# Optimization experiments

Measured on AMD Instinct MI355X. Metric: run time of the kernel, lower is better.

## Reference

```python
import jax, jax.numpy as jnp
import numpy as np

B, N, C = 8, 8192, 512
H, DH = 8, C // 8
SCALE = 0.02


def setup_inputs() -> dict:
    key = jax.random.key(0)
    k0, k1, k2, k3, k4 = jax.random.split(key, 5)
    return {
        "x": jax.random.normal(k0, (B, N, C), dtype=jnp.float32),
        "w1": SCALE * jax.random.normal(k1, (2, H, DH, DH), dtype=jnp.float32),
        "b1": SCALE * jax.random.normal(k2, (2, H, DH), dtype=jnp.float32),
        "w2": SCALE * jax.random.normal(k3, (2, H, DH, DH), dtype=jnp.float32),
        "b2": SCALE * jax.random.normal(k4, (2, H, DH), dtype=jnp.float32),
    }


def reference(x, w1, b1, w2, b2):
    dtype = x.dtype
    x = x.astype(jnp.float32)
    b, n, c = x.shape
    xf = jnp.fft.rfft(x, axis=1, norm="ortho")            # [B, N//2+1, C] complex
    xf = xf.reshape(b, n // 2 + 1, H, DH)                  # [B, F, H, DH]
    xr, xi = jnp.real(xf), jnp.imag(xf)
    # per-head complex linear 1 + GELU (complex mult split into real/imag)
    o1r = jax.nn.gelu(
        jnp.einsum("bfhi,hio->bfho", xr, w1[0])
        - jnp.einsum("bfhi,hio->bfho", xi, w1[1]) + b1[0], approximate=False)
    o1i = jax.nn.gelu(
        jnp.einsum("bfhi,hio->bfho", xi, w1[0])
        + jnp.einsum("bfhi,hio->bfho", xr, w1[1]) + b1[1], approximate=False)
    # per-head complex linear 2
    o2r = (jnp.einsum("bfhi,hio->bfho", o1r, w2[0])
           - jnp.einsum("bfhi,hio->bfho", o1i, w2[1]) + b2[0])
    o2i = (jnp.einsum("bfhi,hio->bfho", o1i, w2[0])
           + jnp.einsum("bfhi,hio->bfho", o1r, w2[1]) + b2[1])
    yf = (o2r + 1j * o2i).reshape(b, n // 2 + 1, c)
    y = jnp.fft.irfft(yf, n=n, axis=1, norm="ortho")
    return y.astype(dtype)
```

## Files before the change

### kernel.cpp

```cpp
#include <hip/hip_runtime.h>
#include <math.h>

#define BB    8
#define NLEN  8192
#define CC    512
#define HH    8
#define DH    64
#define MH    4096
#define FREQ  4097
#define FP    4160
#define NSEQ  (BB*CC)

#define REGION_BYTES ((size_t)NSEQ * FP * 4ull)

static __device__ __align__(256) unsigned char g_scratch[2ull * (size_t)NSEQ * FP * 4ull];
__device__ unsigned short g_wprep[8 * 4 * 64 * 64];

typedef __attribute__((ext_vector_type(8))) short bf16x8;
typedef __attribute__((ext_vector_type(4))) float f32x4;
typedef __attribute__((ext_vector_type(4))) unsigned u32x4;

__device__ __forceinline__ f32x4 MFMA(bf16x8 a, bf16x8 b, f32x4 c){
  return __builtin_amdgcn_mfma_f32_16x16x32_bf16(a, b, c, 0, 0, 0);
}

__device__ __forceinline__ unsigned short f2bf(float f){
  unsigned u = __float_as_uint(f);
  return (unsigned short)((u + 0x7fffu + ((u >> 16) & 1u)) >> 16);
}
__device__ __forceinline__ unsigned pack2(float a, float b){
  return (unsigned)f2bf(a) | ((unsigned)f2bf(b) << 16);
}
__device__ __forceinline__ float bflo(unsigned u){ return __uint_as_float(u << 16); }
__device__ __forceinline__ float bfhi(unsigned u){ return __uint_as_float(u & 0xffff0000u); }

__device__ const float C32C[16] = {
  1.f, 0.98078528f, 0.92387953f, 0.83146961f, 0.70710678f, 0.55557023f,
  0.38268343f, 0.19509032f, 0.f, -0.19509032f, -0.38268343f, -0.55557023f,
  -0.70710678f, -0.83146961f, -0.92387953f, -0.98078528f};
__device__ const float C32S[16] = {
  0.f, 0.19509032f, 0.38268343f, 0.55557023f, 0.70710678f, 0.83146961f,
  0.92387953f, 0.98078528f, 1.f, 0.98078528f, 0.92387953f, 0.83146961f,
  0.70710678f, 0.55557023f, 0.38268343f, 0.19509032f};

__device__ __forceinline__ float gelu_fast(float v){
  float x  = v * 0.70710678118654752440f;
  float ax = fabsf(x);
  float t  = __builtin_amdgcn_rcpf(fmaf(0.3275911f, ax, 1.0f));
  float p  = fmaf(fmaf(fmaf(fmaf(1.061405429f, t, -1.453152027f), t,
                            1.421413741f), t, -0.284496736f), t, 0.254829592f);
  float e  = __expf(-x * x);
  float erf_ax = fmaf(-p * t, e, 1.0f);
  float erfx = copysignf(erf_ax, x);
  return 0.5f * v * (1.0f + erfx);
}

__device__ __forceinline__ float2 cadd(float2 a, float2 b){ return make_float2(a.x+b.x, a.y+b.y); }
__device__ __forceinline__ float2 csub(float2 a, float2 b){ return make_float2(a.x-b.x, a.y-b.y); }
__device__ __forceinline__ float2 cmul(float2 a, float2 b){
  return make_float2(fmaf(a.x, b.x, -(a.y*b.y)), fmaf(a.x, b.y, a.y*b.x));
}

__global__ __launch_bounds__(256) void transpose_in_k(const float* __restrict__ in,
                                                      unsigned* __restrict__ out){
  __shared__ float tile[64][33];
  int b  = blockIdx.z;
  int c0 = blockIdx.x * 32;
  int n0 = blockIdx.y * 64;
  int t  = threadIdx.x;
  int tx = t & 31, ty = t >> 5;
  const float* src = in + ((size_t)b * NLEN + n0) * CC + c0;
  #pragma unroll
  for (int k = 0; k < 8; ++k)
    tile[ty + 8*k][tx] = src[(size_t)(ty + 8*k) * CC + tx];
  __syncthreads();
  int lt = t & 15;
  int nl = 4 * lt;
  #pragma unroll
  for (int kk = 0; kk < 2; ++kk){
    int cl = (t >> 4) + 16*kk;
    uint2 u;
    u.x = pack2(tile[nl    ][cl], tile[nl + 1][cl]);
    u.y = pack2(tile[nl + 2][cl], tile[nl + 3][cl]);
    *(uint2*)(out + ((size_t)(b * CC + c0 + cl) * NLEN + n0) / 2 + 2*lt) = u;
  }
}

__global__ __launch_bounds__(256) void transpose_out_k(const unsigned* __restrict__ in,
                                                       float* __restrict__ out){
  __shared__ float tile[64][33];
  int b  = blockIdx.z;
  int c0 = blockIdx.x * 32;
  int n0 = blockIdx.y * 64;
  int t  = threadIdx.x;
  int lt = t & 15;
  int nl = 4 * lt;
  #pragma unroll
  for (int kk = 0; kk < 2; ++kk){
    int cl = (t >> 4) + 16*kk;
    uint2 u = *(const uint2*)(in + ((size_t)(b * CC + c0 + cl) * NLEN + n0) / 2 + 2*lt);
    tile[nl    ][cl] = bflo(u.x);
    tile[nl + 1][cl] = bfhi(u.x);
    tile[nl + 2][cl] = bflo(u.y);
    tile[nl + 3][cl] = bfhi(u.y);
  }
  __syncthreads();
  int tx = t & 31, ty = t >> 5;
  float* dst = out + ((size_t)b * NLEN + n0) * CC + c0;
  #pragma unroll
  for (int k = 0; k < 8; ++k)
    dst[(size_t)(ty + 8*k) * CC + tx] = tile[ty + 8*k][tx];
}

#define SL(e) ((e) + ((e) >> 4))
#define PERM16(p) ((((p) & 3) << 2) | ((p) >> 2))

template<int SIGN>
__device__ __forceinline__ void dft4ip(float2& v0, float2& v1, float2& v2, float2& v3){
  float2 s02 = cadd(v0, v2), d02 = csub(v0, v2);
  float2 s13 = cadd(v1, v3), d13 = csub(v1, v3);
  float2 id = make_float2(-(float)SIGN * d13.y, (float)SIGN * d13.x);
  v0 = cadd(s02, s13);
  v1 = cadd(d02, id);
  v2 = csub(s02, s13);
  v3 = csub(d02, id);
}

template<int SIGN>
__device__ __forceinline__ float2 w16c(int m){
  const float c1 = 0.9238795325112867f, s1 = 0.3826834323650898f, r = 0.7071067811865476f;
  float cs = 1.f, sn = 0.f;
  if (m == 1){ cs = c1;  sn = s1; }
  else if (m == 2){ cs = r;   sn = r; }
  else if (m == 3){ cs = s1;  sn = c1; }
  else if (m == 4){ cs = 0.f; sn = 1.f; }
  else if (m == 6){ cs = -r;  sn = r; }
  else if (m == 9){ cs = -c1; sn = -s1; }
  return make_float2(cs, (float)SIGN * sn);
}

template<int SIGN>
__device__ __forceinline__ void dft16ip(float2 v[16]){
  #pragma unroll
  for (int q0 = 0; q0 < 4; ++q0) dft4ip<SIGN>(v[q0], v[q0+4], v[q0+8], v[q0+12]);
  #pragma unroll
  for (int p0 = 0; p0 < 4; ++p0)
    #pragma unroll
    for (int q0 = 0; q0 < 4; ++q0){
      const int m = p0 * q0;
      if (m) v[q0 + 4*p0] = cmul(v[q0 + 4*p0], w16c<SIGN>(m));
    }
  #pragma unroll
  for (int p0 = 0; p0 < 4; ++p0) dft4ip<SIGN>(v[4*p0], v[4*p0+1], v[4*p0+2], v[4*p0+3]);
}

template<int SIGN>
__device__ __forceinline__ void twiddle16(float2 v[16], int jm, float invRNs){
  float ang = (float)SIGN * 6.2831853071795864769f * (float)jm * invRNs;
  float sn, cs; __sincosf(ang, &sn, &cs);
  float2 tw[16];
  tw[1] = make_float2(cs, sn);
  #pragma unroll
  for (int q = 2; q < 16; ++q) tw[q] = cmul(tw[q >> 1], tw[q - (q >> 1)]);
  #pragma unroll
  for (int q = 1; q < 16; ++q) v[q] = cmul(v[q], tw[q]);
}

template<int SIGN, int NS>
__device__ __forceinline__ void fft_mid_pass(float2* lds2, float2 v[16], int t){
  #pragma unroll
  for (int q = 0; q < 16; ++q) v[q] = lds2[SL(t + 256*q)];
  int jm = t & (NS - 1);
  if (NS > 1) twiddle16<SIGN>(v, jm, 1.0f / (16.0f * (float)NS));
  dft16ip<SIGN>(v);
  __syncthreads();
  int base = ((t - jm) << 4) + jm;
  #pragma unroll
  for (int p = 0; p < 16; ++p) lds2[SL(base + p*NS)] = v[PERM16(p)];
  __syncthreads();
}

#define ORTHO_S 0.011048543456039806f

__global__ __launch_bounds__(256) void fft_fwd_k(const unsigned* __restrict__ xt,
                                                 unsigned* __restrict__ spec){
  __shared__ float2 lds2[4352];
  int t = threadIdx.x;
  size_t row = blockIdx.x;
  const unsigned* src = xt + row * (NLEN/2);
  float2 v[16];
  #pragma unroll
  for (int q = 0; q < 16; ++q){
    unsigned u = src[t + 256*q];
    v[q] = make_float2(bflo(u), bfhi(u));
  }
  dft16ip<-1>(v);
  #pragma unroll
  for (int p = 0; p < 16; ++p) lds2[SL(16*t + p)] = v[PERM16(p)];
  __syncthreads();
  fft_mid_pass<-1, 16 >(lds2, v, t);
  fft_mid_pass<-1, 256>(lds2, v, t);
  unsigned* dst = spec + row * (size_t)FP;
  float snb, csb;
  __sincosf(-6.2831853071795864769f * (float)t / (float)NLEN, &snb, &csb);
  #pragma unroll
  for (int q = 0; q < 8; ++q){
    int k = t + 256*q;
    float2 zk = lds2[SL(k)];
    float2 zc = lds2[SL((MH - k) & (MH - 1))];
    float ex = 0.5f*(zk.x + zc.x);
    float ey = 0.5f*(zk.y - zc.y);
    float ox =  0.5f*(zk.y + zc.y);
    float oy = -0.5f*(zk.x - zc.x);
    float cs = fmaf(csb, C32C[q],  snb*C32S[q]);
    float sn = fmaf(snb, C32C[q], -csb*C32S[q]);
    float P = cs*ox - sn*oy;
    float Q = cs*oy + sn*ox;
    dst[k]      = pack2(ORTHO_S*(ex + P), ORTHO_S*(ey + Q));
    dst[MH - k] = pack2(ORTHO_S*(ex - P), ORTHO_S*(Q - ey));
  }
  if (t == 0){
    float2 zm = lds2[SL(2048)];
    dst[2048] = pack2(ORTHO_S*zm.x, -ORTHO_S*zm.y);
  }
}

__global__ __launch_bounds__(256) void fft_inv_k(const unsigned* __restrict__ spec,
                                                 unsigned* __restrict__ yt){
  __shared__ float2 lds2[4352];
  int t = threadIdx.x;
  size_t row = blockIdx.x;
  const unsigned* src = spec + row * (size_t)FP;
  float snb, csb;
  __sincosf(6.2831853071795864769f * (float)t / (float)NLEN, &snb, &csb);
  #pragma unroll
  for (int q = 0; q < 8; ++q){
    int k = t + 256*q;
    unsigned uk = src[k];
    unsigned uc = src[MH - k];
    float2 xk = make_float2(bflo(uk), bfhi(uk));
    float2 xc = make_float2(bflo(uc), bfhi(uc));
    if (k == 0){ xk.y = 0.0f; xc.y = 0.0f; }
    float ex = xk.x + xc.x;
    float ey = xk.y - xc.y;
    float dx = xk.x - xc.x;
    float dy = xk.y + xc.y;
    float cs = fmaf(csb, C32C[q], -snb*C32S[q]);
    float sn = fmaf(snb, C32C[q],  csb*C32S[q]);
    float ox = cs*dx - sn*dy;
    float oy = cs*dy + sn*dx;
    lds2[SL(k)] = make_float2(ex - oy, ey + ox);
    if (k > 0)
      lds2[SL(MH - k)] = make_float2(ex + oy, ox - ey);
  }
  if (t == 0){
    unsigned um = src[2048];
    lds2[SL(2048)] = make_float2(2.0f*bflo(um), -2.0f*bfhi(um));
  }
  __syncthreads();
  float2 v[16];
  fft_mid_pass<1, 1  >(lds2, v, t);
  fft_mid_pass<1, 16 >(lds2, v, t);
  fft_mid_pass<1, 256>(lds2, v, t);
  uint4* d4 = (uint4*)(yt + row * (NLEN/2) + 16*t);
  #pragma unroll
  for (int g = 0; g < 4; ++g){
    float2 w0 = lds2[SL(16*t + 4*g    )];
    float2 w1 = lds2[SL(16*t + 4*g + 1)];
    float2 w2 = lds2[SL(16*t + 4*g + 2)];
    float2 w3 = lds2[SL(16*t + 4*g + 3)];
    uint4 stv;
    stv.x = pack2(ORTHO_S*w0.x, ORTHO_S*w0.y);
    stv.y = pack2(ORTHO_S*w1.x, ORTHO_S*w1.y);
    stv.z = pack2(ORTHO_S*w2.x, ORTHO_S*w2.y);
    stv.w = pack2(ORTHO_S*w3.x, ORTHO_S*w3.y);
    d4[g] = stv;
  }
}

__global__ __launch_bounds__(256) void wprep_k(const float* __restrict__ w1,
                                               const float* __restrict__ w2){
  int t = threadIdx.x;
  int h = blockIdx.x;
  #pragma unroll 4
  for (int u = 0; u < 64; ++u){
    int idx = t + 256*u;
    int p = idx >> 12;
    int o = (idx >> 6) & 63;
    int jj = idx & 63;
    int swo = (o ^ (o >> 3)) & 7;
    int s = (((jj >> 3) ^ swo) << 3) | (jj & 7);
    int i;
    if (p < 2){
      i = s;
    } else {
      int ks = s >> 5, g = (s >> 3) & 3, j = s & 7;
      i = (2*ks + (j >> 2))*16 + 4*g + (j & 3);
    }
    const float* src = (p < 2) ? w1 : w2;
    float v = src[(size_t)(p & 1) * 32768 + (size_t)h * 4096 + i * 64 + o];
    g_wprep[(size_t)h * 16384 + idx] = f2bf(v);
  }
}

__global__ __launch_bounds__(256) void afno_mid_mfma_k(const unsigned* __restrict__ spec_in,
                                                       unsigned* __restrict__ spec_out,
                                                       const float* __restrict__ b1,
                                                       const float* __restrict__ b2){
  __shared__ unsigned short Wl[16384];
  const int t = threadIdx.x;
  const int bx = blockIdx.x, h = blockIdx.y, b = blockIdx.z;
  const int F0 = bx * 64;
  const size_t rowbase = ((size_t)b * HH + h) * DH;
  const int l = t & 63, wv = t >> 6;
  const int lf = l & 15, lg = l >> 4;
  const int wf0 = wv * 16;

  int f = F0 + wf0 + lf;
  int fc = (f < FP) ? f : (FP - 1);
  const unsigned* xcol = spec_in + rowbase * (size_t)FP + fc;
  unsigned bins[16];
  #pragma unroll
  for (int ks = 0; ks < 2; ++ks){
    int i0 = (ks*4 + lg) * 8;
    #pragma unroll
    for (int j = 0; j < 8; ++j)
      bins[ks*8 + j] = xcol[(i0 + j) * FP];
  }

  {
    const uint4* gw  = (const uint4*)(g_wprep + (size_t)h * 16384);
    uint4*       sw4 = (uint4*)Wl;
    #pragma unroll
    for (int u = 0; u < 8; ++u) sw4[t + 256*u] = gw[t + 256*u];
  }
  float4 br1[4], bi1[4];
  #pragma unroll
  for (int mt = 0; mt < 4; ++mt){
    br1[mt] = *(const float4*)(b1 +       (size_t)h*64 + mt*16 + lg*4);
    bi1[mt] = *(const float4*)(b1 + 512 + (size_t)h*64 + mt*16 + lg*4);
  }
  float b2r[4], b2i[4];
  #pragma unroll
  for (int nt = 0; nt < 4; ++nt){
    b2r[nt] = b2[(size_t)h*64 + nt*16 + lf];
    b2i[nt] = b2[512 + (size_t)h*64 + nt*16 + lf];
  }
  __syncthreads();

  const unsigned short* W1R = Wl;
  const unsigned short* W1I = Wl + 4096;
  const unsigned short* W2R = Wl + 8192;
  const unsigned short* W2I = Wl + 12288;
  const f32x4 zz = {0.f, 0.f, 0.f, 0.f};

  f32x4 a1R[4], a1I[4];
  #pragma unroll
  for (int mt = 0; mt < 4; ++mt){ a1R[mt] = zz; a1I[mt] = zz; }

  #pragma unroll
  for (int ks = 0; ks < 2; ++ks){
    u32x4 pr, pi;
    pr.x = __builtin_amdgcn_perm(bins[ks*8+1], bins[ks*8+0], 0x05040100u);
    pr.y = __builtin_amdgcn_perm(bins[ks*8+3], bins[ks*8+2], 0x05040100u);
    pr.z = __builtin_amdgcn_perm(bins[ks*8+5], bins[ks*8+4], 0x05040100u);
    pr.w = __builtin_amdgcn_perm(bins[ks*8+7], bins[ks*8+6], 0x05040100u);
    pi.x = __builtin_amdgcn_perm(bins[ks*8+1], bins[ks*8+0], 0x07060302u);
    pi.y = __builtin_amdgcn_perm(bins[ks*8+3], bins[ks*8+2], 0x07060302u);
    pi.z = __builtin_amdgcn_perm(bins[ks*8+5], bins[ks*8+4], 0x07060302u);
    pi.w = __builtin_amdgcn_perm(bins[ks*8+7], bins[ks*8+6], 0x07060302u);
    bf16x8 bxr = __builtin_bit_cast(bf16x8, pr);
    bf16x8 bxi = __builtin_bit_cast(bf16x8, pi);
    int b0 = ks*4 + lg;
    #pragma unroll
    for (int mt = 0; mt < 4; ++mt){
      int o = mt*16 + lf;
      int swo = (o ^ (o >> 3)) & 7;
      int off = o*64 + ((b0 ^ swo) << 3);
      bf16x8 awr  = *(const bf16x8*)(W1R + off);
      bf16x8 awi  = *(const bf16x8*)(W1I + off);
      bf16x8 awin = awi ^ (short)0x8000;
      a1R[mt] = MFMA(awr,  bxr, a1R[mt]);
      a1R[mt] = MFMA(awin, bxi, a1R[mt]);
      a1I[mt] = MFMA(awi,  bxr, a1I[mt]);
      a1I[mt] = MFMA(awr,  bxi, a1I[mt]);
    }
  }

  bf16x8 aFr[2], aFi[2], aFin[2];
  #pragma unroll
  for (int ks = 0; ks < 2; ++ks){
    const int m0 = 2*ks, m1 = 2*ks + 1;
    u32x4 wr4, wi4;
    wr4.x = pack2(gelu_fast(a1R[m0][0] + br1[m0].x), gelu_fast(a1R[m0][1] + br1[m0].y));
    wr4.y = pack2(gelu_fast(a1R[m0][2] + br1[m0].z), gelu_fast(a1R[m0][3] + br1[m0].w));
    wr4.z = pack2(gelu_fast(a1R[m1][0] + br1[m1].x), gelu_fast(a1R[m1][1] + br1[m1].y));
    wr4.w = pack2(gelu_fast(a1R[m1][2] + br1[m1].z), gelu_fast(a1R[m1][3] + br1[m1].w));
    wi4.x = pack2(gelu_fast(a1I[m0][0] + bi1[m0].x), gelu_fast(a1I[m0][1] + bi1[m0].y));
    wi4.y = pack2(gelu_fast(a1I[m0][2] + bi1[m0].z), gelu_fast(a1I[m0][3] + bi1[m0].w));
    wi4.z = pack2(gelu_fast(a1I[m1][0] + bi1[m1].x), gelu_fast(a1I[m1][1] + bi1[m1].y));
    wi4.w = pack2(gelu_fast(a1I[m1][2] + bi1[m1].z), gelu_fast(a1I[m1][3] + bi1[m1].w));
    aFr[ks]  = __builtin_bit_cast(bf16x8, wr4);
    aFi[ks]  = __builtin_bit_cast(bf16x8, wi4);
    aFin[ks] = aFi[ks] ^ (short)0x8000;
  }

  f32x4 a2R[4], a2I[4];
  #pragma unroll
  for (int nt = 0; nt < 4; ++nt){ a2R[nt] = zz; a2I[nt] = zz; }
  #pragma unroll
  for (int ks = 0; ks < 2; ++ks){
    int b0 = ks*4 + lg;
    #pragma unroll
    for (int nt = 0; nt < 4; ++nt){
      int o2 = nt*16 + lf;
      int swo = (o2 ^ (o2 >> 3)) & 7;
      int off = o2*64 + ((b0 ^ swo) << 3);
      bf16x8 bwr = *(const bf16x8*)(W2R + off);
      bf16x8 bwi = *(const bf16x8*)(W2I + off);
      a2R[nt] = MFMA(aFr[ks],  bwr, a2R[nt]);
      a2R[nt] = MFMA(aFin[ks], bwi, a2R[nt]);
      a2I[nt] = MFMA(aFi[ks],  bwr, a2I[nt]);
      a2I[nt] = MFMA(aFr[ks],  bwi, a2I[nt]);
    }
  }

  int f0 = F0 + wf0 + lg*4;
  if (f0 <= MH){
    #pragma unroll
    for (int nt = 0; nt < 4; ++nt){
      int o2 = nt*16 + lf;
      uint4 st;
      st.x = pack2(a2R[nt][0] + b2r[nt], a2I[nt][0] + b2i[nt]);
      st.y = pack2(a2R[nt][1] + b2r[nt], a2I[nt][1] + b2i[nt]);
      st.z = pack2(a2R[nt][2] + b2r[nt], a2I[nt][2] + b2i[nt]);
      st.w = pack2(a2R[nt][3] + b2r[nt], a2I[nt][3] + b2i[nt]);
      *(uint4*)(spec_out + (rowbase + o2) * (size_t)FP + f0) = st;
    }
  }
}

extern "C" void kernel_launch(void* const* d_in, const int* in_sizes, int n_in,
                              void* d_out, int out_size, void* d_ws, size_t ws_size,
                              hipStream_t stream) {
  const float* x  = (const float*)d_in[0];
  const float* w1 = (const float*)d_in[1];
  const float* b1 = (const float*)d_in[2];
  const float* w2 = (const float*)d_in[3];
  const float* b2 = (const float*)d_in[4];
  float* out = (float*)d_out;

  unsigned char* base = (unsigned char*)d_ws;
  if (ws_size < 2 * REGION_BYTES){
    void* p = nullptr;
    hipGetSymbolAddress(&p, HIP_SYMBOL(g_scratch));
    base = (unsigned char*)p;
  }
  unsigned* specA = (unsigned*)base;
  unsigned char* regB = base + REGION_BYTES;
  unsigned* xt    = (unsigned*)regB;
  unsigned* specB = (unsigned*)regB;
  unsigned* ytp   = (unsigned*)base;

  wprep_k<<<8, 256, 0, stream>>>(w1, w2);
  transpose_in_k<<<dim3(CC/32, NLEN/64, BB), 256, 0, stream>>>(x, xt);
  fft_fwd_k<<<NSEQ, 256, 0, stream>>>(xt, specA);
  afno_mid_mfma_k<<<dim3(65, HH, BB), 256, 0, stream>>>(specA, specB, b1, b2);
  fft_inv_k<<<NSEQ, 256, 0, stream>>>(specB, ytp);
  transpose_out_k<<<dim3(CC/32, NLEN/64, BB), 256, 0, stream>>>(ytp, out);
}
```

Measured before the change: 208.4 us.

## Tile spectrum layout into 64x64 frequency-channel blocks per batch-head

Changes the intermediate spectrum layout from row-major [channel][freq] with padded stride to a blocked layout where each batch-head holds 65 tiles of 64 channels by 64 frequencies, contiguous. The mid MFMA kernel then reads and writes each tile as one contiguous 16KB block instead of strided columns across 64 rows, which should improve coalescing and cache locality. The FFT kernels now scatter/gather with 64-element contiguous runs spaced 16KB apart, which may make their global access less sequential.

Result: no change. 205.5 us (-1.4%).

```diff
diff --git a/kernel.cpp b/kernel.cpp
--- a/kernel.cpp
+++ b/kernel.cpp
@@ -10,6 +10,9 @@
 #define FREQ  4097
 #define FP    4160
 #define NSEQ  (BB*CC)
+#define BHSZ  (65*4096)
+
+#define KADDR(k) ((((k) >> 6) << 12) + ((k) & 63))
 
 #define REGION_BYTES ((size_t)NSEQ * FP * 4ull)
 
@@ -200,7 +203,7 @@
   __syncthreads();
   fft_mid_pass<-1, 16 >(lds2, v, t);
   fft_mid_pass<-1, 256>(lds2, v, t);
-  unsigned* dst = spec + row * (size_t)FP;
+  unsigned* dst = spec + (row >> 6) * (size_t)BHSZ + (row & 63) * 64;
   float snb, csb;
   __sincosf(-6.2831853071795864769f * (float)t / (float)NLEN, &snb, &csb);
   #pragma unroll
@@ -216,12 +219,12 @@
     float sn = fmaf(snb, C32C[q], -csb*C32S[q]);
     float P = cs*ox - sn*oy;
     float Q = cs*oy + sn*ox;
-    dst[k]      = pack2(ORTHO_S*(ex + P), ORTHO_S*(ey + Q));
-    dst[MH - k] = pack2(ORTHO_S*(ex - P), ORTHO_S*(Q - ey));
+    dst[KADDR(k)]      = pack2(ORTHO_S*(ex + P), ORTHO_S*(ey + Q));
+    dst[KADDR(MH - k)] = pack2(ORTHO_S*(ex - P), ORTHO_S*(Q - ey));
   }
   if (t == 0){
     float2 zm = lds2[SL(2048)];
-    dst[2048] = pack2(ORTHO_S*zm.x, -ORTHO_S*zm.y);
+    dst[KADDR(2048)] = pack2(ORTHO_S*zm.x, -ORTHO_S*zm.y);
   }
 }
 
@@ -230,14 +233,14 @@
   __shared__ float2 lds2[4352];
   int t = threadIdx.x;
   size_t row = blockIdx.x;
-  const unsigned* src = spec + row * (size_t)FP;
+  const unsigned* src = spec + (row >> 6) * (size_t)BHSZ + (row & 63) * 64;
   float snb, csb;
   __sincosf(6.2831853071795864769f * (float)t / (float)NLEN, &snb, &csb);
   #pragma unroll
   for (int q = 0; q < 8; ++q){
     int k = t + 256*q;
-    unsigned uk = src[k];
-    unsigned uc = src[MH - k];
+    unsigned uk = src[KADDR(k)];
+    unsigned uc = src[KADDR(MH - k)];
     float2 xk = make_float2(bflo(uk), bfhi(uk));
     float2 xc = make_float2(bflo(uc), bfhi(uc));
     if (k == 0){ xk.y = 0.0f; xc.y = 0.0f; }
@@ -254,7 +257,7 @@
       lds2[SL(MH - k)] = make_float2(ex + oy, ox - ey);
   }
   if (t == 0){
-    unsigned um = src[2048];
+    unsigned um = src[KADDR(2048)];
     lds2[SL(2048)] = make_float2(2.0f*bflo(um), -2.0f*bfhi(um));
   }
   __syncthreads();
@@ -310,22 +313,19 @@
   __shared__ unsigned short Wl[16384];
   const int t = threadIdx.x;
   const int bx = blockIdx.x, h = blockIdx.y, b = blockIdx.z;
-  const int F0 = bx * 64;
-  const size_t rowbase = ((size_t)b * HH + h) * DH;
+  const size_t bhoff = (size_t)(b * HH + h) * BHSZ + (size_t)bx * 4096;
   const int l = t & 63, wv = t >> 6;
   const int lf = l & 15, lg = l >> 4;
   const int wf0 = wv * 16;
 
-  int f = F0 + wf0 + lf;
-  int fc = (f < FP) ? f : (FP - 1);
-  const unsigned* xcol = spec_in + rowbase * (size_t)FP + fc;
+  const unsigned* xblk = spec_in + bhoff;
   unsigned bins[16];
   #pragma unroll
   for (int ks = 0; ks < 2; ++ks){
     int i0 = (ks*4 + lg) * 8;
     #pragma unroll
     for (int j = 0; j < 8; ++j)
-      bins[ks*8 + j] = xcol[(i0 + j) * FP];
+      bins[ks*8 + j] = xblk[(i0 + j)*64 + wf0 + lf];
   }
 
   {
@@ -425,18 +425,17 @@
     }
   }
 
-  int f0 = F0 + wf0 + lg*4;
-  if (f0 <= MH){
-    #pragma unroll
-    for (int nt = 0; nt < 4; ++nt){
-      int o2 = nt*16 + lf;
-      uint4 st;
-      st.x = pack2(a2R[nt][0] + b2r[nt], a2I[nt][0] + b2i[nt]);
-      st.y = pack2(a2R[nt][1] + b2r[nt], a2I[nt][1] + b2i[nt]);
-      st.z = pack2(a2R[nt][2] + b2r[nt], a2I[nt][2] + b2i[nt]);
-      st.w = pack2(a2R[nt][3] + b2r[nt], a2I[nt][3] + b2i[nt]);
-      *(uint4*)(spec_out + (rowbase + o2) * (size_t)FP + f0) = st;
-    }
+  unsigned* oblk = spec_out + bhoff;
+  int fl0 = wf0 + lg*4;
+  #pragma unroll
+  for (int nt = 0; nt < 4; ++nt){
+    int o2 = nt*16 + lf;
+    uint4 st;
+    st.x = pack2(a2R[nt][0] + b2r[nt], a2I[nt][0] + b2i[nt]);
+    st.y = pack2(a2R[nt][1] + b2r[nt], a2I[nt][1] + b2i[nt]);
+    st.z = pack2(a2R[nt][2] + b2r[nt], a2I[nt][2] + b2i[nt]);
+    st.w = pack2(a2R[nt][3] + b2r[nt], a2I[nt][3] + b2i[nt]);
+    *(uint4*)(oblk + o2*64 + fl0) = st;
   }
 }
 
```
